# Optimization experiments

Hardware: AMD Instinct MI355X
Metric: run time of the kernel (lower is better)

## Reference

```python
import jax, jax.numpy as jnp
import numpy as np

H = 16  # number of heads

def setup_inputs() -> dict:
    key = jax.random.key(0)
    ks = jax.random.split(key, 9)
    B, N, D = 2, 2048, 1024
    s = 0.02
    q = jax.random.normal(ks[0], (B, N, D), jnp.float32)
    k = jax.random.normal(ks[1], (B, N, D), jnp.float32)
    v = jax.random.normal(ks[2], (B, N, D), jnp.float32)
    mask = jax.random.randint(ks[3], (B, 1, N, N), 0, 2).astype(bool)
    Wq = jax.random.normal(ks[4], (D, D), jnp.float32) * s
    Wk = jax.random.normal(ks[5], (D, D), jnp.float32) * s
    Wv = jax.random.normal(ks[6], (D, D), jnp.float32) * s
    Wo = jax.random.normal(ks[7], (D, D), jnp.float32) * s
    bq = jnp.zeros((D,), jnp.float32)
    bk = jnp.zeros((D,), jnp.float32)
    bv = jnp.zeros((D,), jnp.float32)
    bo = jnp.zeros((D,), jnp.float32)
    return {"q": q, "k": k, "v": v, "mask": mask,
            "Wq": Wq, "bq": bq, "Wk": Wk, "bk": bk,
            "Wv": Wv, "bv": bv, "Wo": Wo, "bo": bo}


def reference(q, k, v, mask, Wq, bq, Wk, bk, Wv, bv, Wo, bo):
    B, N, D = q.shape
    dk = D // H
    # nn.Linear: x @ W.T + b, then split heads: b n (h d) -> b h n d
    def proj(x, W, b):
        return (x @ W.T + b).reshape(B, N, H, dk).transpose(0, 2, 1, 3)
    qh = proj(q, Wq, bq)  # [B,H,N,dk]
    kh = proj(k, Wk, bk)
    vh = proj(v, Wv, bv)
    # NOTE: original has NO 1/sqrt(dk) scaling
    score = jnp.einsum('bhnd,bhmd->bhnm', qh, kh)
    score = jnp.where(mask, jnp.float32(-1e9), score)
    attn = jax.nn.softmax(score, axis=-1)
    x = jnp.einsum('bhnm,bhmd->bhnd', attn, vh)
    x = x.transpose(0, 2, 1, 3).reshape(B, N, D)  # b h n d -> b n (h d)
    return x @ Wo.T + bo
```

## Files before the change

### kernel.cpp

```cpp
#include <hip/hip_runtime.h>
#include <math.h>

#define BB 2
#define NN 2048
#define DD 1024
#define HH 16
#define DK 64
#define LOG2E 1.4426950408889634f

typedef __attribute__((ext_vector_type(8))) short short8;
typedef __attribute__((ext_vector_type(4))) float f32x4;
typedef __attribute__((ext_vector_type(16))) float f32x16;
typedef __attribute__((ext_vector_type(4))) float f32x4v;
typedef __attribute__((ext_vector_type(8))) unsigned short ushort8;
typedef __attribute__((ext_vector_type(4))) unsigned short ushort4v;
typedef unsigned long long u64;

__device__ __forceinline__ unsigned short f2bf(float f) {
  unsigned u = __float_as_uint(f);
  unsigned r = (u + 0x7FFFu + ((u >> 16) & 1u)) >> 16;
  return (unsigned short)r;
}

__device__ __forceinline__ unsigned cvtpk(float a, float b) {
  unsigned r;
  asm("v_cvt_pk_bf16_f32 %0, %1, %2" : "=v"(r) : "v"(a), "v"(b));
  return r;
}

__device__ __forceinline__ void gload_lds16(const void* g, void* l) {
  auto gp = (const __attribute__((address_space(1))) unsigned int*)(unsigned long long)g;
  auto lp = (__attribute__((address_space(3))) unsigned int*)(unsigned int)(unsigned long long)l;
  __builtin_amdgcn_global_load_lds(gp, lp, 16, 0, 0);
}

__global__ __launch_bounds__(256) void cvt_w(
    const float* __restrict__ wq, const float* __restrict__ wk, const float* __restrict__ wv,
    const float* __restrict__ wo, unsigned short* __restrict__ ws)
{
  const long NW = (long)DD * DD;
  long i = ((long)blockIdx.x * blockDim.x + threadIdx.x) * 8;
  if (i >= 4 * NW) return;
  int s = (int)(i / NW);
  const float* src = (s == 0) ? wq : (s == 1) ? wk : (s == 2) ? wv : wo;
  long off = i - (long)s * NW;
  unsigned short* dst = ws + (long)s * NW + off;
  f32x4v a = *(const f32x4v*)(src + off);
  f32x4v b = *(const f32x4v*)(src + off + 4);
  ushort8 o;
  o[0] = f2bf(a[0]); o[1] = f2bf(a[1]); o[2] = f2bf(a[2]); o[3] = f2bf(a[3]);
  o[4] = f2bf(b[0]); o[5] = f2bf(b[1]); o[6] = f2bf(b[2]); o[7] = f2bf(b[3]);
  *(ushort8*)dst = o;
}

__global__ __launch_bounds__(256) void cvt_mask_bits(const void* __restrict__ mask,
                                                     u64* __restrict__ mb, long total64)
{
  const unsigned char* m8 = (const unsigned char*)mask;
  const int l = threadIdx.x & 63;
  unsigned probe = m8[l * 4 + 1] | m8[l * 4 + 2] | m8[l * 4 + 3];
  const bool isBool = (__any(probe != 0) != 0);

  long t = (long)blockIdx.x * blockDim.x + threadIdx.x;
  if (t >= total64) return;
  u64 bits = 0;
  if (isBool) {
    const uint4* p = (const uint4*)(m8 + t * 64);
#pragma unroll
    for (int i = 0; i < 4; ++i) {
      uint4 q4 = p[i];
      unsigned vv[4] = {q4.x, q4.y, q4.z, q4.w};
#pragma unroll
      for (int j = 0; j < 4; ++j)
#pragma unroll
        for (int bb = 0; bb < 4; ++bb)
          bits |= (u64)((vv[j] >> (8 * bb)) & 1u) << (i * 16 + j * 4 + bb);
    }
  } else {
    const int4* p = (const int4*)((const int*)mask + t * 64);
#pragma unroll
    for (int i = 0; i < 16; ++i) {
      int4 q4 = p[i];
      bits |= (u64)(q4.x & 1) << (i * 4);
      bits |= (u64)(q4.y & 1) << (i * 4 + 1);
      bits |= (u64)(q4.z & 1) << (i * 4 + 2);
      bits |= (u64)(q4.w & 1) << (i * 4 + 3);
    }
  }
  const long bb2 = t >> 16;
  const long qq = (t >> 5) & 2047;
  const long tcol = t & 31;
  mb[(bb2 * 32 + tcol) * 2048 + qq] = bits;
}

struct GemmArgs {
  const void* A;
  const unsigned short* Bw;
  const float* bias;
  void* C;
  int mode;
  float oscale;
};

template<int TM, int BN, int AFP32>
__global__ __launch_bounds__(256) void gemm_bt(GemmArgs ga0, GemmArgs ga1, GemmArgs ga2)
{
  constexpr int K = DD;
  constexpr int Nn = DD;
  constexpr int GX = 1024 / BN;
  constexpr int GY = 4096 / TM;
  constexpr int PERZ = GX * GY;
  constexpr int MF = TM / 32;
  constexpr int NF = BN / 32;
  constexpr int NT = K / 32;
  __shared__ __align__(16) unsigned short As[3][TM * 32];
  __shared__ __align__(16) unsigned short Bs[3][BN * 32];

  int wgid = blockIdx.x + (blockIdx.y + blockIdx.z * GY) * GX;
  const int nwg = (int)gridDim.z * PERZ;
  const int chunk = nwg >> 3;
  wgid = (wgid & 7) * chunk + (wgid >> 3);
  const int zi = wgid / PERZ;
  const int rem = wgid % PERZ;
  const int m0 = (rem / GX) * TM;
  const int n0 = (rem % GX) * BN;
  GemmArgs ga = (zi == 0) ? ga0 : ((zi == 1) ? ga1 : ga2);

  const int tid = threadIdx.x;
  const int lane = tid & 63;
  const int w = tid >> 6;
  const int m_woff = (w >> 1) * (TM / 2);
  const int n_woff = (w & 1) * (BN / 2);
  const int c = lane & 15, g = lane >> 4;

  f32x4 acc[MF][NF];
  const f32x4 z4 = {0.f, 0.f, 0.f, 0.f};
#pragma unroll
  for (int m = 0; m < MF; ++m)
#pragma unroll
    for (int n = 0; n < NF; ++n) acc[m][n] = z4;

  const unsigned short* Bb = ga.Bw + (long)n0 * K;
  const int ar = tid >> 2;
  const int ac = ((tid & 3) ^ (ar & 3)) * 8;

  auto STAGE_B = [&](int buf, int kk) {
#pragma unroll
    for (int i = 0; i < BN / 64; ++i)
      gload_lds16(Bb + (long)(i * 64 + ar) * K + kk + ac, &Bs[buf][i * 2048 + tid * 8]);
  };

  const unsigned short* Ab16 = (const unsigned short*)ga.A + (long)m0 * K;
  const int arow = tid >> 1;
  const int ahalf = tid & 1;
  const float* Afp = (const float*)ga.A + (long)(m0 + arow) * K + ahalf * 16;
  f32x4v aregA[4], aregB[4];

  auto STAGE_A16 = [&](int buf, int kk) {
#pragma unroll
    for (int i = 0; i < TM / 64; ++i)
      gload_lds16(Ab16 + (long)(i * 64 + ar) * K + kk + ac, &As[buf][i * 2048 + tid * 8]);
  };
  auto LOAD_A = [&](int kk, f32x4v (&arr)[4]) {
#pragma unroll
    for (int j = 0; j < 4; ++j) arr[j] = *(const f32x4v*)(Afp + kk + 4 * j);
  };
  auto WRITE_A = [&](int buf, f32x4v (&arr)[4]) {
    union { short8 s; unsigned u[4]; } p0, p1;
    p0.u[0] = cvtpk(arr[0][0], arr[0][1]); p0.u[1] = cvtpk(arr[0][2], arr[0][3]);
    p0.u[2] = cvtpk(arr[1][0], arr[1][1]); p0.u[3] = cvtpk(arr[1][2], arr[1][3]);
    p1.u[0] = cvtpk(arr[2][0], arr[2][1]); p1.u[1] = cvtpk(arr[2][2], arr[2][3]);
    p1.u[2] = cvtpk(arr[3][0], arr[3][1]); p1.u[3] = cvtpk(arr[3][2], arr[3][3]);
    const int fa = ((arow & 1) << 1) | ((arow >> 1) & 1);
    const int G0 = (2 * ahalf) ^ fa;
    const int G1 = (2 * ahalf + 1) ^ fa;
    *(short8*)((char*)&As[buf][0] + arow * 64 + G0 * 16) = p0.s;
    *(short8*)((char*)&As[buf][0] + arow * 64 + G1 * 16) = p1.s;
  };

  if constexpr (AFP32) {
    LOAD_A(0, aregA);
    LOAD_A(32, aregB);
    STAGE_B(0, 0);
    STAGE_B(1, 32);
    WRITE_A(0, aregA);
    LOAD_A(64, aregA);
  } else {
    STAGE_A16(0, 0);
    STAGE_B(0, 0);
    STAGE_A16(1, 32);
    STAGE_B(1, 32);
  }

  const int rswz = (g ^ (c & 3)) * 8;
  const int aswz = AFP32 ? (g ^ (((c & 1) << 1) | ((c >> 1) & 1))) * 8
                         : rswz;

  auto ITER = [&](int t, f32x4v (&bank)[4]) {
    if constexpr (AFP32) {
      if (t < NT - 2)       asm volatile("s_waitcnt vmcnt(6) lgkmcnt(0)" ::: "memory");
      else if (t == NT - 2) asm volatile("s_waitcnt vmcnt(2) lgkmcnt(0)" ::: "memory");
      else                  asm volatile("s_waitcnt vmcnt(0) lgkmcnt(0)" ::: "memory");
    } else {
      constexpr int LPS = TM / 64 + BN / 64;
      if (t < NT - 1) {
        if constexpr (LPS == 4) asm volatile("s_waitcnt vmcnt(4)" ::: "memory");
        else                    asm volatile("s_waitcnt vmcnt(3)" ::: "memory");
      } else {
        asm volatile("s_waitcnt vmcnt(0)" ::: "memory");
      }
    }
    __builtin_amdgcn_s_barrier();
    __builtin_amdgcn_sched_barrier(0);

    if constexpr (AFP32) {
      if (t + 1 < NT) WRITE_A((t + 1) % 3, bank);
      if (t + 3 < NT) LOAD_A((t + 3) * 32, bank);
      if (t + 2 < NT) STAGE_B((t + 2) % 3, (t + 2) * 32);
    } else {
      if (t + 2 < NT) { STAGE_A16((t + 2) % 3, (t + 2) * 32); STAGE_B((t + 2) % 3, (t + 2) * 32); }
    }

    const int cb = t % 3;
    short8 a[MF], b[NF];
#pragma unroll
    for (int m = 0; m < MF; ++m)
      a[m] = *(const short8*)&As[cb][(m_woff + 16 * m + c) * 32 + aswz];
#pragma unroll
    for (int n = 0; n < NF; ++n)
      b[n] = *(const short8*)&Bs[cb][(n_woff + 16 * n + c) * 32 + rswz];
    __builtin_amdgcn_s_setprio(1);
#pragma unroll
    for (int m = 0; m < MF; ++m)
#pragma unroll
      for (int n = 0; n < NF; ++n)
        acc[m][n] = __builtin_amdgcn_mfma_f32_16x16x32_bf16(a[m], b[n], acc[m][n], 0, 0, 0);
    __builtin_amdgcn_s_setprio(0);
  };

  for (int t = 0; t < NT; t += 2) {
    ITER(t, aregB);
    ITER(t + 1, aregA);
  }

#pragma unroll
  for (int n = 0; n < NF; ++n) {
    const int col = n0 + n_woff + 16 * n + c;
    const float bv = ga.bias[col];
#pragma unroll
    for (int m = 0; m < MF; ++m) {
      const int row0 = m0 + m_woff + 16 * m + 4 * g;
      if (ga.mode == 2) {
        ushort4v pk;
#pragma unroll
        for (int r = 0; r < 4; ++r) pk[r] = f2bf((acc[m][n][r] + bv) * ga.oscale);
        *(ushort4v*)&((unsigned short*)ga.C)[((long)(row0 >> 11) * DD + col) * NN + (row0 & (NN - 1))] = pk;
      } else {
#pragma unroll
        for (int r = 0; r < 4; ++r) {
          const int row = row0 + r;
          const float val = (acc[m][n][r] + bv) * ga.oscale;
          if (ga.mode == 1)
            ((float*)ga.C)[(long)row * Nn + col] = val;
          else
            ((unsigned short*)ga.C)[(long)row * Nn + col] = f2bf(val);
        }
      }
    }
  }
}

__global__ __launch_bounds__(512) void attn_kernel(
    const unsigned short* __restrict__ Q,
    const unsigned short* __restrict__ K,
    const unsigned short* __restrict__ Vt,
    const u64* __restrict__ mb64,
    unsigned short* __restrict__ ctx)
{
  __shared__ __align__(16) char lds_raw[65536];
  unsigned short* KsB = (unsigned short*)lds_raw;
  unsigned short* VsB = (unsigned short*)(lds_raw + 32768);
  float* OB = (float*)lds_raw;

  const int tid = threadIdx.x;
  const int lane = tid & 63;
  const int w = tid >> 6;
  const int grp = w >> 2;
  const int wq = w & 3;
  const int bid = blockIdx.x;
  const int b = (bid >> 4) & 1, h = bid & 15;
  const int q0 = (bid >> 5) * 128;
  const int l31 = lane & 31;
  const int hi = lane >> 5;
  const int qrow = q0 + 32 * wq + l31;

  short8 aq[4];
  {
    const unsigned short* qp = Q + ((long)(b * NN + qrow)) * DD + h * DK + 8 * hi;
    aq[0] = *(const short8*)(qp);
    aq[1] = *(const short8*)(qp + 16);
    aq[2] = *(const short8*)(qp + 32);
    aq[3] = *(const short8*)(qp + 48);
  }

  f32x16 o0, o1, cinit;
#pragma unroll
  for (int r = 0; r < 16; ++r) { o0[r] = 0.f; o1[r] = 0.f; cinit[r] = -28.853901f; }
  float ls0 = 0.f, ls1 = 0.f;

  const unsigned short* Kbase = K + (long)(b * NN) * DD + h * DK;
  const unsigned short* Vbase = Vt + ((long)(b * DD + h * DK)) * NN;
  const u64* mbase = mb64 + (long)(b * 32) * 2048 + qrow;

  const int srow = tid >> 3;
  const int scol = tid & 7;
  const int swcol = scol ^ (srow & 7);

  auto STAGE = [&](int buf, int t) {
    gload_lds16(Kbase + (long)(t * 64 + srow) * DD + swcol * 8, &KsB[buf * 4096 + tid * 8]);
    gload_lds16(Vbase + (long)srow * NN + t * 64 + swcol * 8, &VsB[buf * 4096 + tid * 8]);
    gload_lds16(Kbase + (long)((t + 16) * 64 + srow) * DD + swcol * 8, &KsB[(2 + buf) * 4096 + tid * 8]);
    gload_lds16(Vbase + (long)srow * NN + (t + 16) * 64 + swcol * 8, &VsB[(2 + buf) * 4096 + tid * 8]);
  };

  int koffs[8], voff0[4], voff1[4];
#pragma unroll
  for (int sub = 0; sub < 2; ++sub) {
    const int krow = l31 + 32 * sub;
    const int kswz = (l31 & 7) << 3;
#pragma unroll
    for (int i = 0; i < 4; ++i)
      koffs[sub * 4 + i] = krow * 64 + ((16 * i + 8 * hi) ^ kswz);
#pragma unroll
    for (int dblk = 0; dblk < 2; ++dblk) {
      const int vrow = l31 + 32 * dblk;
      voff0[sub * 2 + dblk] = vrow * 64 + ((32 * sub + 8 * hi) ^ kswz);
      voff1[sub * 2 + dblk] = vrow * 64 + ((32 * sub + 16 + 8 * hi) ^ kswz);
    }
  }

  STAGE(0, 0);
  __syncthreads();
  int cur = 0;
  const int sh4 = 4 * hi;
  u64 mword = mbase[(long)(grp * 16) * 2048];

  for (int t = 0; t < 16; ++t) {
    const int tt = grp * 16 + t;
    const u64 mnext = (t < 15) ? mbase[(long)(tt + 1) * 2048] : 0;
    if (t < 15) STAGE(cur ^ 1, t + 1);
    const unsigned msk0 = ((unsigned)mword) >> sh4;
    const unsigned msk1 = ((unsigned)(mword >> 32)) >> sh4;
    const unsigned short* Kt = &KsB[(grp * 2 + cur) * 4096];
    const unsigned short* Vtl = &VsB[(grp * 2 + cur) * 4096];

#pragma unroll
    for (int sub = 0; sub < 2; ++sub) {
      const unsigned m = sub ? msk1 : msk0;

      f32x16 ss = cinit;
      __builtin_amdgcn_s_setprio(1);
#pragma unroll
      for (int i = 0; i < 4; ++i) {
        const short8 kf = *(const short8*)&Kt[koffs[sub * 4 + i]];
        ss = __builtin_amdgcn_mfma_f32_32x32x16_bf16(kf, aq[i], ss, 0, 0, 0);
      }
      __builtin_amdgcn_s_setprio(0);

      unsigned wv[8];
      float lacc = 0.f;
#pragma unroll
      for (int i = 0; i < 8; ++i) {
        const int r0 = 2 * i, r1 = 2 * i + 1;
        const int cr0 = (r0 & 3) + 8 * (r0 >> 2);
        const int cr1 = (r1 & 3) + 8 * (r1 >> 2);
        const float e0 = ((m >> cr0) & 1u) ? -1e9f : ss[r0];
        const float e1 = ((m >> cr1) & 1u) ? -1e9f : ss[r1];
        const float p0 = __builtin_amdgcn_exp2f(e0);
        const float p1 = __builtin_amdgcn_exp2f(e1);
        lacc += p0 + p1;
        wv[i] = cvtpk(p0, p1);
      }
      if (sub == 0) ls0 += lacc; else ls1 += lacc;

      asm("v_permlane32_swap_b32 %0, %1" : "+v"(wv[0]), "+v"(wv[2]));
      asm("v_permlane32_swap_b32 %0, %1" : "+v"(wv[1]), "+v"(wv[3]));
      asm("v_permlane32_swap_b32 %0, %1" : "+v"(wv[4]), "+v"(wv[6]));
      asm("v_permlane32_swap_b32 %0, %1" : "+v"(wv[5]), "+v"(wv[7]));
      union { short8 s; unsigned u[4]; } pa0, pa1;
      pa0.u[0] = wv[0]; pa0.u[1] = wv[1]; pa0.u[2] = wv[2]; pa0.u[3] = wv[3];
      pa1.u[0] = wv[4]; pa1.u[1] = wv[5]; pa1.u[2] = wv[6]; pa1.u[3] = wv[7];

      __builtin_amdgcn_s_setprio(1);
      {
        const short8 vb00 = *(const short8*)&Vtl[voff0[sub * 2 + 0]];
        const short8 vb10 = *(const short8*)&Vtl[voff1[sub * 2 + 0]];
        o0 = __builtin_amdgcn_mfma_f32_32x32x16_bf16(pa0.s, vb00, o0, 0, 0, 0);
        o0 = __builtin_amdgcn_mfma_f32_32x32x16_bf16(pa1.s, vb10, o0, 0, 0, 0);
        const short8 vb01 = *(const short8*)&Vtl[voff0[sub * 2 + 1]];
        const short8 vb11 = *(const short8*)&Vtl[voff1[sub * 2 + 1]];
        o1 = __builtin_amdgcn_mfma_f32_32x32x16_bf16(pa0.s, vb01, o1, 0, 0, 0);
        o1 = __builtin_amdgcn_mfma_f32_32x32x16_bf16(pa1.s, vb11, o1, 0, 0, 0);
      }
      __builtin_amdgcn_s_setprio(0);
    }
    __syncthreads();
    cur ^= 1;
    mword = mnext;
  }

  float lsum = ls0 + ls1;
  const int li = wq * 64 + lane;
  if (grp == 1) {
    float* dst = OB + (long)li * 33;
#pragma unroll
    for (int r = 0; r < 16; ++r) { dst[r] = o0[r]; dst[16 + r] = o1[r]; }
    dst[32] = lsum;
  }
  __syncthreads();
  if (grp == 0) {
    const float* src = OB + (long)li * 33;
#pragma unroll
    for (int r = 0; r < 16; ++r) { o0[r] += src[r]; o1[r] += src[16 + r]; }
    lsum += src[32];
    lsum += __shfl_xor(lsum, 32);
    const float inv = 1.0f / lsum;

#pragma unroll
    for (int r = 0; r < 16; ++r) {
      const int qr = (r & 3) + 8 * (r >> 2) + 4 * hi;
      const float linv = __shfl(inv, qr);
      const long row = (long)(b * NN + q0 + 32 * wq + qr);
      ctx[row * DD + h * DK + l31] = f2bf(o0[r] * linv);
      ctx[row * DD + h * DK + 32 + l31] = f2bf(o1[r] * linv);
    }
  }
}

extern "C" void kernel_launch(void* const* d_in, const int* in_sizes, int n_in,
                              void* d_out, int out_size, void* d_ws, size_t ws_size,
                              hipStream_t stream) {
  const float* q  = (const float*)d_in[0];
  const float* k  = (const float*)d_in[1];
  const float* v  = (const float*)d_in[2];
  const void*  mask = d_in[3];
  const float* Wq = (const float*)d_in[4];
  const float* bq = (const float*)d_in[5];
  const float* Wk = (const float*)d_in[6];
  const float* bk = (const float*)d_in[7];
  const float* Wv = (const float*)d_in[8];
  const float* bv = (const float*)d_in[9];
  const float* Wo = (const float*)d_in[10];
  const float* bo = (const float*)d_in[11];

  unsigned short* ws = (unsigned short*)d_ws;
  const long NW = (long)DD * DD;
  const long NX = (long)BB * NN * DD;
  unsigned short* Wqb = ws;
  unsigned short* Wkb = ws + NW;
  unsigned short* Wvb = ws + 2 * NW;
  unsigned short* Wob = ws + 3 * NW;
  unsigned short* Qh  = ws + 4 * NW;
  unsigned short* Kh  = Qh + NX;
  unsigned short* Vtr = Kh + NX;
  unsigned short* Ctx = Vtr + NX;
  u64* Mbits = (u64*)(Ctx + NX);
  const long NM64 = (long)BB * NN * NN / 64;

  cvt_w<<<2048, 256, 0, stream>>>(Wq, Wk, Wv, Wo, ws);
  cvt_mask_bits<<<(int)(NM64 / 256), 256, 0, stream>>>(mask, Mbits, NM64);

  GemmArgs gq = {q, Wqb, bq, (void*)Qh, 0, LOG2E};
  GemmArgs gk = {k, Wkb, bk, (void*)Kh, 0, 1.0f};
  GemmArgs gv = {v, Wvb, bv, (void*)Vtr, 2, 1.0f};
  dim3 gproj(DD / 128, (BB * NN) / 128, 3);
  gemm_bt<128, 128, 1><<<gproj, 256, 0, stream>>>(gq, gk, gv);

  attn_kernel<<<512, 512, 0, stream>>>(Qh, Kh, Vtr, Mbits, Ctx);

  GemmArgs go = {Ctx, Wob, bo, d_out, 1, 1.0f};
  dim3 gout(DD / 128, (BB * NN) / 64, 1);
  gemm_bt<64, 128, 0><<<gout, 256, 0, stream>>>(go, go, go);
}
```

Before: 136.6 us.

## Pre-convert Q/K/V activations to bf16 in a separate pass before projection GEMM

New measurement: 130.1 us (median of 2 runs). -4.8%, faster.

```diff
diff --git a/kernel.cpp b/kernel.cpp
--- a/kernel.cpp
+++ b/kernel.cpp
@@ -34,17 +34,28 @@
   __builtin_amdgcn_global_load_lds(gp, lp, 16, 0, 0);
 }
 
-__global__ __launch_bounds__(256) void cvt_w(
+__global__ __launch_bounds__(256) void cvt_all(
+    const float* __restrict__ q, const float* __restrict__ k, const float* __restrict__ v,
     const float* __restrict__ wq, const float* __restrict__ wk, const float* __restrict__ wv,
     const float* __restrict__ wo, unsigned short* __restrict__ ws)
 {
   const long NW = (long)DD * DD;
+  const long NX = (long)BB * NN * DD;
   long i = ((long)blockIdx.x * blockDim.x + threadIdx.x) * 8;
-  if (i >= 4 * NW) return;
-  int s = (int)(i / NW);
-  const float* src = (s == 0) ? wq : (s == 1) ? wk : (s == 2) ? wv : wo;
-  long off = i - (long)s * NW;
-  unsigned short* dst = ws + (long)s * NW + off;
+  if (i >= 4 * NW + 3 * NX) return;
+  const float* src; unsigned short* dst; long off;
+  if (i < 4 * NW) {
+    int s = (int)(i / NW);
+    src = (s == 0) ? wq : (s == 1) ? wk : (s == 2) ? wv : wo;
+    off = i - (long)s * NW;
+    dst = ws + (long)s * NW + off;
+  } else {
+    long j = i - 4 * NW;
+    int s = (int)(j / NX);
+    src = (s == 0) ? q : (s == 1) ? k : v;
+    off = j - (long)s * NX;
+    dst = ws + 4 * NW + (long)s * NX + off;
+  }
   f32x4v a = *(const f32x4v*)(src + off);
   f32x4v b = *(const f32x4v*)(src + off + 4);
   ushort8 o;
@@ -94,7 +105,7 @@
 }
 
 struct GemmArgs {
-  const void* A;
+  const unsigned short* A;
   const unsigned short* Bw;
   const float* bias;
   void* C;
@@ -102,7 +113,7 @@
   float oscale;
 };
 
-template<int TM, int BN, int AFP32>
+template<int TM, int BN>
 __global__ __launch_bounds__(256) void gemm_bt(GemmArgs ga0, GemmArgs ga1, GemmArgs ga2)
 {
   constexpr int K = DD;
@@ -113,6 +124,7 @@
   constexpr int MF = TM / 32;
   constexpr int NF = BN / 32;
   constexpr int NT = K / 32;
+  constexpr int LPS = TM / 64 + BN / 64;
   __shared__ __align__(16) unsigned short As[3][TM * 32];
   __shared__ __align__(16) unsigned short Bs[3][BN * 32];
 
@@ -140,92 +152,43 @@
 #pragma unroll
     for (int n = 0; n < NF; ++n) acc[m][n] = z4;
 
+  const unsigned short* Ab = ga.A + (long)m0 * K;
   const unsigned short* Bb = ga.Bw + (long)n0 * K;
   const int ar = tid >> 2;
   const int ac = ((tid & 3) ^ (ar & 3)) * 8;
 
-  auto STAGE_B = [&](int buf, int kk) {
+  auto STAGE = [&](int buf, int kk) {
+#pragma unroll
+    for (int i = 0; i < TM / 64; ++i)
+      gload_lds16(Ab + (long)(i * 64 + ar) * K + kk + ac, &As[buf][i * 2048 + tid * 8]);
 #pragma unroll
     for (int i = 0; i < BN / 64; ++i)
       gload_lds16(Bb + (long)(i * 64 + ar) * K + kk + ac, &Bs[buf][i * 2048 + tid * 8]);
   };
 
-  const unsigned short* Ab16 = (const unsigned short*)ga.A + (long)m0 * K;
-  const int arow = tid >> 1;
-  const int ahalf = tid & 1;
-  const float* Afp = (const float*)ga.A + (long)(m0 + arow) * K + ahalf * 16;
-  f32x4v aregA[4], aregB[4];
-
-  auto STAGE_A16 = [&](int buf, int kk) {
-#pragma unroll
-    for (int i = 0; i < TM / 64; ++i)
-      gload_lds16(Ab16 + (long)(i * 64 + ar) * K + kk + ac, &As[buf][i * 2048 + tid * 8]);
-  };
-  auto LOAD_A = [&](int kk, f32x4v (&arr)[4]) {
-#pragma unroll
-    for (int j = 0; j < 4; ++j) arr[j] = *(const f32x4v*)(Afp + kk + 4 * j);
-  };
-  auto WRITE_A = [&](int buf, f32x4v (&arr)[4]) {
-    union { short8 s; unsigned u[4]; } p0, p1;
-    p0.u[0] = cvtpk(arr[0][0], arr[0][1]); p0.u[1] = cvtpk(arr[0][2], arr[0][3]);
-    p0.u[2] = cvtpk(arr[1][0], arr[1][1]); p0.u[3] = cvtpk(arr[1][2], arr[1][3]);
-    p1.u[0] = cvtpk(arr[2][0], arr[2][1]); p1.u[1] = cvtpk(arr[2][2], arr[2][3]);
-    p1.u[2] = cvtpk(arr[3][0], arr[3][1]); p1.u[3] = cvtpk(arr[3][2], arr[3][3]);
-    const int fa = ((arow & 1) << 1) | ((arow >> 1) & 1);
-    const int G0 = (2 * ahalf) ^ fa;
-    const int G1 = (2 * ahalf + 1) ^ fa;
-    *(short8*)((char*)&As[buf][0] + arow * 64 + G0 * 16) = p0.s;
-    *(short8*)((char*)&As[buf][0] + arow * 64 + G1 * 16) = p1.s;
-  };
-
-  if constexpr (AFP32) {
-    LOAD_A(0, aregA);
-    LOAD_A(32, aregB);
-    STAGE_B(0, 0);
-    STAGE_B(1, 32);
-    WRITE_A(0, aregA);
-    LOAD_A(64, aregA);
-  } else {
-    STAGE_A16(0, 0);
-    STAGE_B(0, 0);
-    STAGE_A16(1, 32);
-    STAGE_B(1, 32);
-  }
+  STAGE(0, 0);
+  STAGE(1, 32);
 
   const int rswz = (g ^ (c & 3)) * 8;
-  const int aswz = AFP32 ? (g ^ (((c & 1) << 1) | ((c >> 1) & 1))) * 8
-                         : rswz;
-
-  auto ITER = [&](int t, f32x4v (&bank)[4]) {
-    if constexpr (AFP32) {
-      if (t < NT - 2)       asm volatile("s_waitcnt vmcnt(6) lgkmcnt(0)" ::: "memory");
-      else if (t == NT - 2) asm volatile("s_waitcnt vmcnt(2) lgkmcnt(0)" ::: "memory");
-      else                  asm volatile("s_waitcnt vmcnt(0) lgkmcnt(0)" ::: "memory");
+
+  for (int t = 0; t < NT; ++t) {
+    if (t < NT - 1) {
+      if constexpr (LPS == 4)
+        asm volatile("s_waitcnt vmcnt(4)" ::: "memory");
+      else
+        asm volatile("s_waitcnt vmcnt(3)" ::: "memory");
     } else {
-      constexpr int LPS = TM / 64 + BN / 64;
-      if (t < NT - 1) {
-        if constexpr (LPS == 4) asm volatile("s_waitcnt vmcnt(4)" ::: "memory");
-        else                    asm volatile("s_waitcnt vmcnt(3)" ::: "memory");
-      } else {
-        asm volatile("s_waitcnt vmcnt(0)" ::: "memory");
-      }
+      asm volatile("s_waitcnt vmcnt(0)" ::: "memory");
     }
     __builtin_amdgcn_s_barrier();
     __builtin_amdgcn_sched_barrier(0);
-
-    if constexpr (AFP32) {
-      if (t + 1 < NT) WRITE_A((t + 1) % 3, bank);
-      if (t + 3 < NT) LOAD_A((t + 3) * 32, bank);
-      if (t + 2 < NT) STAGE_B((t + 2) % 3, (t + 2) * 32);
-    } else {
-      if (t + 2 < NT) { STAGE_A16((t + 2) % 3, (t + 2) * 32); STAGE_B((t + 2) % 3, (t + 2) * 32); }
-    }
+    if (t + 2 < NT) STAGE((t + 2) % 3, (t + 2) * 32);
 
     const int cb = t % 3;
     short8 a[MF], b[NF];
 #pragma unroll
     for (int m = 0; m < MF; ++m)
-      a[m] = *(const short8*)&As[cb][(m_woff + 16 * m + c) * 32 + aswz];
+      a[m] = *(const short8*)&As[cb][(m_woff + 16 * m + c) * 32 + rswz];
 #pragma unroll
     for (int n = 0; n < NF; ++n)
       b[n] = *(const short8*)&Bs[cb][(n_woff + 16 * n + c) * 32 + rswz];
@@ -236,11 +199,6 @@
       for (int n = 0; n < NF; ++n)
         acc[m][n] = __builtin_amdgcn_mfma_f32_16x16x32_bf16(a[m], b[n], acc[m][n], 0, 0, 0);
     __builtin_amdgcn_s_setprio(0);
-  };
-
-  for (int t = 0; t < NT; t += 2) {
-    ITER(t, aregB);
-    ITER(t + 1, aregA);
   }
 
 #pragma unroll
@@ -460,25 +418,28 @@
   unsigned short* Wkb = ws + NW;
   unsigned short* Wvb = ws + 2 * NW;
   unsigned short* Wob = ws + 3 * NW;
-  unsigned short* Qh  = ws + 4 * NW;
+  unsigned short* Xq  = ws + 4 * NW;
+  unsigned short* Xk  = Xq + NX;
+  unsigned short* Xv  = Xk + NX;
+  unsigned short* Qh  = Xv + NX;
   unsigned short* Kh  = Qh + NX;
   unsigned short* Vtr = Kh + NX;
   unsigned short* Ctx = Vtr + NX;
   u64* Mbits = (u64*)(Ctx + NX);
   const long NM64 = (long)BB * NN * NN / 64;
 
-  cvt_w<<<2048, 256, 0, stream>>>(Wq, Wk, Wv, Wo, ws);
+  cvt_all<<<8192, 256, 0, stream>>>(q, k, v, Wq, Wk, Wv, Wo, ws);
   cvt_mask_bits<<<(int)(NM64 / 256), 256, 0, stream>>>(mask, Mbits, NM64);
 
-  GemmArgs gq = {q, Wqb, bq, (void*)Qh, 0, LOG2E};
-  GemmArgs gk = {k, Wkb, bk, (void*)Kh, 0, 1.0f};
-  GemmArgs gv = {v, Wvb, bv, (void*)Vtr, 2, 1.0f};
+  GemmArgs gq = {Xq, Wqb, bq, (void*)Qh, 0, LOG2E};
+  GemmArgs gk = {Xk, Wkb, bk, (void*)Kh, 0, 1.0f};
+  GemmArgs gv = {Xv, Wvb, bv, (void*)Vtr, 2, 1.0f};
   dim3 gproj(DD / 128, (BB * NN) / 128, 3);
-  gemm_bt<128, 128, 1><<<gproj, 256, 0, stream>>>(gq, gk, gv);
+  gemm_bt<128, 128><<<gproj, 256, 0, stream>>>(gq, gk, gv);
 
   attn_kernel<<<512, 512, 0, stream>>>(Qh, Kh, Vtr, Mbits, Ctx);
 
   GemmArgs go = {Ctx, Wob, bo, d_out, 1, 1.0f};
   dim3 gout(DD / 128, (BB * NN) / 64, 1);
-  gemm_bt<64, 128, 0><<<gout, 256, 0, stream>>>(go, go, go);
-}
+  gemm_bt<64, 128><<<gout, 256, 0, stream>>>(go, go, go);
+}
```
